# Kernel tuning notes

Hardware: AMD Instinct MI355X
Metric: run time of the kernel (lower is better)

## Reference

```python
import jax, jax.numpy as jnp
import numpy as np

OHKM_K = 8
STRUCT_WEIGHT = 1.0
# Standard COCO person skeleton (19 edges over 17 keypoints)
COCO_PERSON_SKELETON = np.array([
    (15, 13), (13, 11), (16, 14), (14, 12), (11, 12), (5, 11), (6, 12),
    (5, 6), (5, 7), (6, 8), (7, 9), (8, 10), (1, 2), (0, 1), (0, 2),
    (1, 3), (2, 4), (3, 5), (4, 6)], dtype=np.int32)


def setup_inputs() -> dict:
    key = jax.random.key(0)
    k1, k2, k3, k4, k5 = jax.random.split(key, 5)
    B, K, C_paf, H, W = 32, 17, 38, 128, 128
    return {
        "heatmap_pred": jax.random.normal(k1, (B, K, H, W), dtype=jnp.float32),
        "paf_pred": jax.random.normal(k2, (B, C_paf, H, W), dtype=jnp.float32),
        "heatmap_gt": jax.random.uniform(k3, (B, K, H, W), dtype=jnp.float32),
        "paf_gt": jax.random.normal(k4, (B, C_paf, H, W), dtype=jnp.float32),
        "joint_coords_gt": jax.random.randint(k5, (B, K, 2), 0, 128, dtype=jnp.int32),
    }


def _struct_loss(heatmap_pred, joint_coords_gt):
    # pred coords from heatmap argmax (vectorized replacement of the python loop)
    B, K, H, W = heatmap_pred.shape
    idx = jnp.argmax(heatmap_pred.reshape(B, K, H * W), axis=2)  # [B,K]
    px = (idx % W).astype(jnp.float32)
    py = (idx // W).astype(jnp.float32)
    pred = jnp.stack([px, py], axis=-1)                 # [B,K,2] (x,y)
    gt = joint_coords_gt.astype(jnp.float32)            # [B,K,2]
    edges = jnp.asarray(COCO_PERSON_SKELETON)           # [E,2]
    a, b = edges[:, 0], edges[:, 1]
    pred_len = jnp.sqrt(jnp.sum((pred[:, a] - pred[:, b]) ** 2, axis=-1))  # [B,E]
    gt_len = jnp.sqrt(jnp.sum((gt[:, a] - gt[:, b]) ** 2, axis=-1))        # [B,E]
    E = edges.shape[0]  # count: all edges valid
    per_batch = jnp.sum((pred_len - gt_len) ** 2, axis=1) / (E + 1e-6)
    return jnp.mean(per_batch)


def reference(heatmap_pred, paf_pred, heatmap_gt, paf_gt, joint_coords_gt):
    # OHKM heatmap loss: per-keypoint MSE, top-k hardest per sample, mean
    per_kp_loss = jnp.mean((heatmap_pred - heatmap_gt) ** 2, axis=(2, 3))  # [B,K]
    Kk = min(OHKM_K, per_kp_loss.shape[1])
    topk_vals, _ = jax.lax.top_k(per_kp_loss, Kk)                          # [B,Kk]
    heatmap_loss = jnp.mean(jnp.mean(topk_vals, axis=1))
    paf_loss = jnp.mean((paf_pred - paf_gt) ** 2)
    total = heatmap_loss + paf_loss
    total = total + STRUCT_WEIGHT * _struct_loss(heatmap_pred, joint_coords_gt)
    return total
```

## Files before the change

### kernel.cpp

```cpp
#include <hip/hip_runtime.h>
#include <math.h>

#define B_ 32
#define K_ 17
#define H_ 128
#define W_ 128
#define HW_ (H_ * W_)
#define C_PAF_ 38
#define NE_ 19
#define HM_BLOCKS (B_ * K_)
#define PAF_BLOCKS 1216
#define PAF_ITERS 16
#define THREADS 256
#define PAF_N ((size_t)B_ * C_PAF_ * H_ * W_)
#define PAF_N4 (PAF_N / 4)

__constant__ int c_edge_a[NE_] = {15,13,16,14,11, 5, 6, 5, 5, 6, 7, 8, 1, 0, 0, 1, 2, 3, 4};
__constant__ int c_edge_b[NE_] = {13,11,14,12,12,11,12, 6, 7, 8, 9,10, 2, 1, 2, 3, 4, 5, 6};

__global__ __launch_bounds__(THREADS) void pose_reduce_kernel(
    const float* __restrict__ hm_pred, const float* __restrict__ hm_gt,
    const float* __restrict__ paf_pred, const float* __restrict__ paf_gt,
    float* __restrict__ per_kp, int* __restrict__ amax,
    float* __restrict__ paf_partial)
{
    __shared__ float s_val[4];
    __shared__ float s_ssq[4];
    __shared__ int   s_idx[4];

    const int t = threadIdx.x;
    const int bid = blockIdx.x;
    const int wave = t >> 6;
    const int lane = t & 63;

    if (bid < HM_BLOCKS) {
        const float4* __restrict__ p = (const float4*)(hm_pred + (size_t)bid * HW_);
        const float4* __restrict__ g = (const float4*)(hm_gt   + (size_t)bid * HW_);
        float ssq[4] = {0.0f, 0.0f, 0.0f, 0.0f};
        float m[4]; int mi[4];
        #pragma unroll
        for (int j = 0; j < 4; ++j) { m[j] = -INFINITY; mi[j] = 0; }
        #pragma unroll
        for (int i = 0; i < HW_ / 4 / THREADS; ++i) {
            const int j = i & 3;
            const int v = t + i * THREADS;
            const float4 a = p[v];
            const float4 b = g[v];
            const float d0 = a.x - b.x, d1 = a.y - b.y, d2 = a.z - b.z, d3 = a.w - b.w;
            ssq[j] += d0 * d0 + d1 * d1 + d2 * d2 + d3 * d3;
            float m4 = a.x; int k4 = 0;
            if (a.y > m4) { m4 = a.y; k4 = 1; }
            if (a.z > m4) { m4 = a.z; k4 = 2; }
            if (a.w > m4) { m4 = a.w; k4 = 3; }
            if (m4 > m[j]) { m[j] = m4; mi[j] = 4 * v + k4; }
        }
        float sT = (ssq[0] + ssq[1]) + (ssq[2] + ssq[3]);
        float M = m[0]; int MI = mi[0];
        #pragma unroll
        for (int j = 1; j < 4; ++j)
            if (m[j] > M || (m[j] == M && mi[j] < MI)) { M = m[j]; MI = mi[j]; }
        #pragma unroll
        for (int off = 32; off > 0; off >>= 1) {
            const float m2  = __shfl_down(M,  off);
            const int   mi2 = __shfl_down(MI, off);
            const float s2  = __shfl_down(sT, off);
            sT += s2;
            if (m2 > M || (m2 == M && mi2 < MI)) { M = m2; MI = mi2; }
        }
        if (lane == 0) { s_val[wave] = M; s_idx[wave] = MI; s_ssq[wave] = sT; }
        __syncthreads();
        if (t == 0) {
            #pragma unroll
            for (int wv = 1; wv < 4; ++wv) {
                sT += s_ssq[wv];
                if (s_val[wv] > M || (s_val[wv] == M && s_idx[wv] < MI)) {
                    M = s_val[wv]; MI = s_idx[wv];
                }
            }
            per_kp[bid] = sT * (1.0f / (float)HW_);
            amax[bid] = MI;
        }
    } else {
        const int pb = bid - HM_BLOCKS;
        const float4* __restrict__ p = (const float4*)paf_pred;
        const float4* __restrict__ g = (const float4*)paf_gt;
        const size_t base = (size_t)pb * THREADS + t;
        const size_t stride = (size_t)PAF_BLOCKS * THREADS;
        float ssq[4] = {0.0f, 0.0f, 0.0f, 0.0f};
        #pragma unroll
        for (int i = 0; i < PAF_ITERS; ++i) {
            const size_t idx = base + (size_t)i * stride;
            const float4 a = p[idx];
            const float4 b = g[idx];
            const float d0 = a.x - b.x, d1 = a.y - b.y, d2 = a.z - b.z, d3 = a.w - b.w;
            ssq[i & 3] += d0 * d0 + d1 * d1 + d2 * d2 + d3 * d3;
        }
        float sT = (ssq[0] + ssq[1]) + (ssq[2] + ssq[3]);
        #pragma unroll
        for (int off = 32; off > 0; off >>= 1) sT += __shfl_down(sT, off);
        if (lane == 0) s_ssq[wave] = sT;
        __syncthreads();
        if (t == 0) paf_partial[pb] = (s_ssq[0] + s_ssq[1]) + (s_ssq[2] + s_ssq[3]);
    }
}

__global__ __launch_bounds__(THREADS) void pose_final_kernel(
    const float* __restrict__ per_kp, const int* __restrict__ amax,
    const float* __restrict__ paf_partial, const int* __restrict__ coords,
    float* __restrict__ out)
{
    __shared__ float s_p[4];
    const int t = threadIdx.x;
    const int wave = t >> 6;
    const int lane = t & 63;

    float ps = 0.0f;
    for (int i = t; i < PAF_BLOCKS; i += THREADS) ps += paf_partial[i];
    #pragma unroll
    for (int off = 32; off > 0; off >>= 1) ps += __shfl_down(ps, off);
    if (lane == 0) s_p[wave] = ps;
    __syncthreads();

    float val = 0.0f;
    if (t < B_) {
        const int b = t;
        float lk[K_];
        float px[K_], py[K_];
        #pragma unroll
        for (int k = 0; k < K_; ++k) {
            lk[k] = per_kp[b * K_ + k];
            const int idx = amax[b * K_ + k];
            px[k] = (float)(idx & (W_ - 1));
            py[k] = (float)(idx >> 7);
        }
        float tsum = 0.0f;
        for (int j = 0; j < 8; ++j) {
            int best = 0; float bv = lk[0];
            for (int k = 1; k < K_; ++k) if (lk[k] > bv) { bv = lk[k]; best = k; }
            tsum += bv;
            lk[best] = -INFINITY;
        }
        float s = 0.0f;
        for (int e = 0; e < NE_; ++e) {
            const int ea = c_edge_a[e], eb = c_edge_b[e];
            const float dx = px[ea] - px[eb];
            const float dy = py[ea] - py[eb];
            const float plen = sqrtf(dx * dx + dy * dy);
            const float gax = (float)coords[(b * K_ + ea) * 2];
            const float gay = (float)coords[(b * K_ + ea) * 2 + 1];
            const float gbx = (float)coords[(b * K_ + eb) * 2];
            const float gby = (float)coords[(b * K_ + eb) * 2 + 1];
            const float gx = gax - gbx, gy = gay - gby;
            const float glen = sqrtf(gx * gx + gy * gy);
            const float d = plen - glen;
            s += d * d;
        }
        val = tsum * (1.0f / 8.0f) + s / (19.0f + 1e-6f);
    }
    #pragma unroll
    for (int off = 16; off > 0; off >>= 1) val += __shfl_down(val, off);
    if (t == 0) {
        const float paf_sum = s_p[0] + s_p[1] + s_p[2] + s_p[3];
        out[0] = val * (1.0f / (float)B_) + paf_sum * (1.0f / (float)PAF_N);
    }
}

extern "C" void kernel_launch(void* const* d_in, const int* in_sizes, int n_in,
                              void* d_out, int out_size, void* d_ws, size_t ws_size,
                              hipStream_t stream) {
    const float* hm_pred  = (const float*)d_in[0];
    const float* paf_pred = (const float*)d_in[1];
    const float* hm_gt    = (const float*)d_in[2];
    const float* paf_gt   = (const float*)d_in[3];
    const int*   coords   = (const int*)d_in[4];
    float* out = (float*)d_out;

    float* per_kp      = (float*)d_ws;
    int*   amax        = (int*)((char*)d_ws + HM_BLOCKS * sizeof(float));
    float* paf_partial = (float*)((char*)d_ws + 2 * HM_BLOCKS * sizeof(float));

    pose_reduce_kernel<<<HM_BLOCKS + PAF_BLOCKS, THREADS, 0, stream>>>(
        hm_pred, hm_gt, paf_pred, paf_gt, per_kp, amax, paf_partial);
    pose_final_kernel<<<1, THREADS, 0, stream>>>(
        per_kp, amax, paf_partial, coords, out);
}
```

Measured before the change: 237.9 us.

## Split heatmap tiles across two blocks, use contiguous PAF chunks with nontemporal loads

```diff
diff --git a/kernel.cpp b/kernel.cpp
--- a/kernel.cpp
+++ b/kernel.cpp
@@ -8,21 +8,28 @@
 #define HW_ (H_ * W_)
 #define C_PAF_ 38
 #define NE_ 19
-#define HM_BLOCKS (B_ * K_)
-#define PAF_BLOCKS 1216
-#define PAF_ITERS 16
+#define HM_TILES (B_ * K_)
+#define HM_BLOCKS (HM_TILES * 2)
+#define HM_HALF 8192
+#define PAF_BLOCKS 2432
 #define THREADS 256
 #define PAF_N ((size_t)B_ * C_PAF_ * H_ * W_)
 #define PAF_N4 (PAF_N / 4)
 
+typedef float fvec4 __attribute__((ext_vector_type(4)));
+
 __constant__ int c_edge_a[NE_] = {15,13,16,14,11, 5, 6, 5, 5, 6, 7, 8, 1, 0, 0, 1, 2, 3, 4};
 __constant__ int c_edge_b[NE_] = {13,11,14,12,12,11,12, 6, 7, 8, 9,10, 2, 1, 2, 3, 4, 5, 6};
 
-__global__ __launch_bounds__(THREADS) void pose_reduce_kernel(
+#define WS_SSQH 0
+#define WS_MH   (HM_BLOCKS)
+#define WS_MIH  (2 * HM_BLOCKS)
+#define WS_PAF  (3 * HM_BLOCKS)
+
+__global__ __launch_bounds__(THREADS, 8) void pose_reduce_kernel(
     const float* __restrict__ hm_pred, const float* __restrict__ hm_gt,
     const float* __restrict__ paf_pred, const float* __restrict__ paf_gt,
-    float* __restrict__ per_kp, int* __restrict__ amax,
-    float* __restrict__ paf_partial)
+    float* __restrict__ ws_f, int* __restrict__ ws_i)
 {
     __shared__ float s_val[4];
     __shared__ float s_ssq[4];
@@ -34,36 +41,52 @@
     const int lane = t & 63;
 
     if (bid < HM_BLOCKS) {
-        const float4* __restrict__ p = (const float4*)(hm_pred + (size_t)bid * HW_);
-        const float4* __restrict__ g = (const float4*)(hm_gt   + (size_t)bid * HW_);
-        float ssq[4] = {0.0f, 0.0f, 0.0f, 0.0f};
-        float m[4]; int mi[4];
-        #pragma unroll
-        for (int j = 0; j < 4; ++j) { m[j] = -INFINITY; mi[j] = 0; }
-        #pragma unroll
-        for (int i = 0; i < HW_ / 4 / THREADS; ++i) {
-            const int j = i & 3;
-            const int v = t + i * THREADS;
-            const float4 a = p[v];
-            const float4 b = g[v];
-            const float d0 = a.x - b.x, d1 = a.y - b.y, d2 = a.z - b.z, d3 = a.w - b.w;
-            ssq[j] += d0 * d0 + d1 * d1 + d2 * d2 + d3 * d3;
-            float m4 = a.x; int k4 = 0;
-            if (a.y > m4) { m4 = a.y; k4 = 1; }
-            if (a.z > m4) { m4 = a.z; k4 = 2; }
-            if (a.w > m4) { m4 = a.w; k4 = 3; }
-            if (m4 > m[j]) { m[j] = m4; mi[j] = 4 * v + k4; }
-        }
-        float sT = (ssq[0] + ssq[1]) + (ssq[2] + ssq[3]);
-        float M = m[0]; int MI = mi[0];
-        #pragma unroll
-        for (int j = 1; j < 4; ++j)
-            if (m[j] > M || (m[j] == M && mi[j] < MI)) { M = m[j]; MI = mi[j]; }
-        #pragma unroll
-        for (int off = 32; off > 0; off >>= 1) {
-            const float m2  = __shfl_down(M,  off);
-            const int   mi2 = __shfl_down(MI, off);
-            const float s2  = __shfl_down(sT, off);
+        const int tile = bid >> 1;
+        const int half = bid & 1;
+        const size_t off = (size_t)tile * HW_ + (size_t)half * HM_HALF;
+        const fvec4* __restrict__ p = (const fvec4*)(hm_pred + off);
+        const fvec4* __restrict__ g = (const fvec4*)(hm_gt   + off);
+        float ssq[2] = {0.0f, 0.0f};
+        float m[2] = {-INFINITY, -INFINITY};
+        int mi[2] = {0, 0};
+        #pragma unroll
+        for (int ob = 0; ob < 4; ++ob) {
+            const int v0 = t + (ob * 2 + 0) * THREADS;
+            const int v1 = t + (ob * 2 + 1) * THREADS;
+            const fvec4 a0 = __builtin_nontemporal_load(p + v0);
+            const fvec4 b0 = __builtin_nontemporal_load(g + v0);
+            const fvec4 a1 = __builtin_nontemporal_load(p + v1);
+            const fvec4 b1 = __builtin_nontemporal_load(g + v1);
+            {
+                const float d0 = a0.x - b0.x, d1 = a0.y - b0.y;
+                const float d2 = a0.z - b0.z, d3 = a0.w - b0.w;
+                ssq[0] += d0 * d0 + d1 * d1 + d2 * d2 + d3 * d3;
+                float m4 = a0.x; int k4 = 0;
+                if (a0.y > m4) { m4 = a0.y; k4 = 1; }
+                if (a0.z > m4) { m4 = a0.z; k4 = 2; }
+                if (a0.w > m4) { m4 = a0.w; k4 = 3; }
+                if (m4 > m[0]) { m[0] = m4; mi[0] = 4 * v0 + k4; }
+            }
+            {
+                const float d0 = a1.x - b1.x, d1 = a1.y - b1.y;
+                const float d2 = a1.z - b1.z, d3 = a1.w - b1.w;
+                ssq[1] += d0 * d0 + d1 * d1 + d2 * d2 + d3 * d3;
+                float m4 = a1.x; int k4 = 0;
+                if (a1.y > m4) { m4 = a1.y; k4 = 1; }
+                if (a1.z > m4) { m4 = a1.z; k4 = 2; }
+                if (a1.w > m4) { m4 = a1.w; k4 = 3; }
+                if (m4 > m[1]) { m[1] = m4; mi[1] = 4 * v1 + k4; }
+            }
+        }
+        float sT = ssq[0] + ssq[1];
+        float M; int MI;
+        if (m[1] > m[0] || (m[1] == m[0] && mi[1] < mi[0])) { M = m[1]; MI = mi[1]; }
+        else { M = m[0]; MI = mi[0]; }
+        #pragma unroll
+        for (int off2 = 32; off2 > 0; off2 >>= 1) {
+            const float m2  = __shfl_down(M,  off2);
+            const int   mi2 = __shfl_down(MI, off2);
+            const float s2  = __shfl_down(sT, off2);
             sT += s2;
             if (m2 > M || (m2 == M && mi2 < MI)) { M = m2; MI = mi2; }
         }
@@ -77,37 +100,46 @@
                     M = s_val[wv]; MI = s_idx[wv];
                 }
             }
-            per_kp[bid] = sT * (1.0f / (float)HW_);
-            amax[bid] = MI;
+            ws_f[WS_SSQH + bid] = sT;
+            ws_f[WS_MH + bid] = M;
+            ws_i[WS_MIH + bid] = half * HM_HALF + MI;
         }
     } else {
         const int pb = bid - HM_BLOCKS;
-        const float4* __restrict__ p = (const float4*)paf_pred;
-        const float4* __restrict__ g = (const float4*)paf_gt;
-        const size_t base = (size_t)pb * THREADS + t;
-        const size_t stride = (size_t)PAF_BLOCKS * THREADS;
-        float ssq[4] = {0.0f, 0.0f, 0.0f, 0.0f};
-        #pragma unroll
-        for (int i = 0; i < PAF_ITERS; ++i) {
-            const size_t idx = base + (size_t)i * stride;
-            const float4 a = p[idx];
-            const float4 b = g[idx];
-            const float d0 = a.x - b.x, d1 = a.y - b.y, d2 = a.z - b.z, d3 = a.w - b.w;
-            ssq[i & 3] += d0 * d0 + d1 * d1 + d2 * d2 + d3 * d3;
-        }
-        float sT = (ssq[0] + ssq[1]) + (ssq[2] + ssq[3]);
-        #pragma unroll
-        for (int off = 32; off > 0; off >>= 1) sT += __shfl_down(sT, off);
+        const fvec4* __restrict__ p = (const fvec4*)paf_pred + (size_t)pb * 2048;
+        const fvec4* __restrict__ g = (const fvec4*)paf_gt   + (size_t)pb * 2048;
+        float ssq[2] = {0.0f, 0.0f};
+        #pragma unroll
+        for (int ob = 0; ob < 4; ++ob) {
+            const int v0 = t + (ob * 2 + 0) * THREADS;
+            const int v1 = t + (ob * 2 + 1) * THREADS;
+            const fvec4 a0 = __builtin_nontemporal_load(p + v0);
+            const fvec4 b0 = __builtin_nontemporal_load(g + v0);
+            const fvec4 a1 = __builtin_nontemporal_load(p + v1);
+            const fvec4 b1 = __builtin_nontemporal_load(g + v1);
+            {
+                const float d0 = a0.x - b0.x, d1 = a0.y - b0.y;
+                const float d2 = a0.z - b0.z, d3 = a0.w - b0.w;
+                ssq[0] += d0 * d0 + d1 * d1 + d2 * d2 + d3 * d3;
+            }
+            {
+                const float d0 = a1.x - b1.x, d1 = a1.y - b1.y;
+                const float d2 = a1.z - b1.z, d3 = a1.w - b1.w;
+                ssq[1] += d0 * d0 + d1 * d1 + d2 * d2 + d3 * d3;
+            }
+        }
+        float sT = ssq[0] + ssq[1];
+        #pragma unroll
+        for (int off2 = 32; off2 > 0; off2 >>= 1) sT += __shfl_down(sT, off2);
         if (lane == 0) s_ssq[wave] = sT;
         __syncthreads();
-        if (t == 0) paf_partial[pb] = (s_ssq[0] + s_ssq[1]) + (s_ssq[2] + s_ssq[3]);
+        if (t == 0) ws_f[WS_PAF + pb] = (s_ssq[0] + s_ssq[1]) + (s_ssq[2] + s_ssq[3]);
     }
 }
 
 __global__ __launch_bounds__(THREADS) void pose_final_kernel(
-    const float* __restrict__ per_kp, const int* __restrict__ amax,
-    const float* __restrict__ paf_partial, const int* __restrict__ coords,
-    float* __restrict__ out)
+    const float* __restrict__ ws_f, const int* __restrict__ ws_i,
+    const int* __restrict__ coords, float* __restrict__ out)
 {
     __shared__ float s_p[4];
     const int t = threadIdx.x;
@@ -115,7 +147,7 @@
     const int lane = t & 63;
 
     float ps = 0.0f;
-    for (int i = t; i < PAF_BLOCKS; i += THREADS) ps += paf_partial[i];
+    for (int i = t; i < PAF_BLOCKS; i += THREADS) ps += ws_f[WS_PAF + i];
     #pragma unroll
     for (int off = 32; off > 0; off >>= 1) ps += __shfl_down(ps, off);
     if (lane == 0) s_p[wave] = ps;
@@ -128,13 +160,16 @@
         float px[K_], py[K_];
         #pragma unroll
         for (int k = 0; k < K_; ++k) {
-            lk[k] = per_kp[b * K_ + k];
-            const int idx = amax[b * K_ + k];
+            const int j = b * K_ + k;
+            const float s0 = ws_f[WS_SSQH + 2 * j], s1 = ws_f[WS_SSQH + 2 * j + 1];
+            lk[k] = (s0 + s1) * (1.0f / (float)HW_);
+            const float m0 = ws_f[WS_MH + 2 * j], m1 = ws_f[WS_MH + 2 * j + 1];
+            const int idx = (m1 > m0) ? ws_i[WS_MIH + 2 * j + 1] : ws_i[WS_MIH + 2 * j];
             px[k] = (float)(idx & (W_ - 1));
             py[k] = (float)(idx >> 7);
         }
         float tsum = 0.0f;
-        for (int j = 0; j < 8; ++j) {
+        for (int jj = 0; jj < 8; ++jj) {
             int best = 0; float bv = lk[0];
             for (int k = 1; k < K_; ++k) if (lk[k] > bv) { bv = lk[k]; best = k; }
             tsum += bv;
@@ -175,12 +210,10 @@
     const int*   coords   = (const int*)d_in[4];
     float* out = (float*)d_out;
 
-    float* per_kp      = (float*)d_ws;
-    int*   amax        = (int*)((char*)d_ws + HM_BLOCKS * sizeof(float));
-    float* paf_partial = (float*)((char*)d_ws + 2 * HM_BLOCKS * sizeof(float));
+    float* ws_f = (float*)d_ws;
+    int*   ws_i = (int*)d_ws;
 
     pose_reduce_kernel<<<HM_BLOCKS + PAF_BLOCKS, THREADS, 0, stream>>>(
-        hm_pred, hm_gt, paf_pred, paf_gt, per_kp, amax, paf_partial);
-    pose_final_kernel<<<1, THREADS, 0, stream>>>(
-        per_kp, amax, paf_partial, coords, out);
+        hm_pred, hm_gt, paf_pred, paf_gt, ws_f, ws_i);
+    pose_final_kernel<<<1, THREADS, 0, stream>>>(ws_f, ws_i, coords, out);
 }
```

Result: faster. 213.5 us, median of 2 (-10.2%).
